# Kernel optimization log

Hardware: AMD Instinct MI355X
Metric: run time of the kernel (lower is better)

## Reference

```python
import jax, jax.numpy as jnp
import numpy as np

N_NODES = 100000


def gcn_conv(x, edge_index, W, b, n_nodes):
    # PyG GCNConv: add self-loops, symmetric normalization D^-1/2 (A+I) D^-1/2, then XW + b
    xw = x @ W  # [N, out]
    loops = jnp.arange(n_nodes, dtype=edge_index.dtype)
    src = jnp.concatenate([edge_index[0], loops])  # [E+N]
    dst = jnp.concatenate([edge_index[1], loops])
    deg = jax.ops.segment_sum(jnp.ones_like(dst, dtype=xw.dtype), dst, num_segments=n_nodes)
    dinv = jnp.where(deg > 0, deg ** -0.5, 0.0).astype(xw.dtype)
    norm = dinv[src] * dinv[dst]  # [E+N]
    msgs = xw[src] * norm[:, None]  # gather source features, scale
    out = jax.ops.segment_sum(msgs, dst, num_segments=n_nodes)  # scatter-add at dst
    return out + b


def setup_inputs() -> dict:
    key = jax.random.key(0)
    k1, k2, k3, k4 = jax.random.split(key, 4)
    F_in, dim, n_cls, n_edges = 512, 32, 40, 3200000
    x = jax.random.normal(k1, (N_NODES, F_in), dtype=jnp.float32)
    edge_index = jax.random.randint(k2, (2, n_edges), 0, N_NODES, dtype=jnp.int64)
    W1 = jax.random.normal(k3, (F_in, dim), dtype=jnp.float32) * (1.0 / np.sqrt(F_in))
    b1 = jnp.zeros((dim,), dtype=jnp.float32)
    W2 = jax.random.normal(k4, (dim, n_cls), dtype=jnp.float32) * (1.0 / np.sqrt(dim))
    b2 = jnp.zeros((n_cls,), dtype=jnp.float32)
    return {"x": x, "edge_index": edge_index, "W1": W1, "b1": b1, "W2": W2, "b2": b2}


def reference(x, edge_index, W1, b1, W2, b2):
    h = jax.nn.relu(gcn_conv(x, edge_index, W1, b1, N_NODES))
    # F.dropout with training=False (eval) is identity
    logits = gcn_conv(h, edge_index, W2, b2, N_NODES)
    return jax.nn.log_softmax(logits, axis=1)
```

## Files before the change

### kernel.cpp

```cpp
#include <hip/hip_runtime.h>
#include <hip/hip_bf16.h>
#include <math.h>


#define DIM 32
#define NCLS 40
#define F_IN 512
#define BSH 8
#define EPB 8192

__device__ __forceinline__ unsigned int bf16rne(float x) {
    unsigned int u = __float_as_uint(x);
    return (u + 0x7fffu + ((u >> 16) & 1u)) >> 16;
}
__device__ __forceinline__ unsigned int packpair(float lo, float hi) {
    return bf16rne(lo) | (bf16rne(hi) << 16);
}
__device__ __forceinline__ void unpack8(uint4 u, float* f) {
    f[0] = __uint_as_float(u.x << 16);
    f[1] = __uint_as_float(u.x & 0xffff0000u);
    f[2] = __uint_as_float(u.y << 16);
    f[3] = __uint_as_float(u.y & 0xffff0000u);
    f[4] = __uint_as_float(u.z << 16);
    f[5] = __uint_as_float(u.z & 0xffff0000u);
    f[6] = __uint_as_float(u.w << 16);
    f[7] = __uint_as_float(u.w & 0xffff0000u);
}

__global__ __launch_bounds__(256) void hist_k(const int* __restrict__ dst,
                                              int* __restrict__ gh, int E, int nbk) {
    __shared__ int h[512];
    int tid = threadIdx.x;
    h[tid] = 0; h[tid + 256] = 0;
    __syncthreads();
    int base = blockIdx.x * EPB;
#pragma unroll 4
    for (int k = 0; k < EPB / 256; ++k) {
        int e = base + k * 256 + tid;
        if (e < E) atomicAdd(&h[dst[e] >> BSH], 1);
    }
    __syncthreads();
    if (h[tid]) atomicAdd(&gh[tid], h[tid]);
    if (h[tid + 256]) atomicAdd(&gh[tid + 256], h[tid + 256]);
}

__global__ __launch_bounds__(512) void scanb_k(const int* __restrict__ gh,
                                               int* __restrict__ bbase,
                                               int* __restrict__ gcur, int nbk) {
    __shared__ int sh[512];
    int t = threadIdx.x;
    int c = (t < nbk) ? gh[t] : 0;
    sh[t] = c;
    __syncthreads();
    for (int off = 1; off < 512; off <<= 1) {
        int v = sh[t];
        if (t >= off) v += sh[t - off];
        __syncthreads();
        sh[t] = v;
        __syncthreads();
    }
    int excl = sh[t] - c;
    if (t < nbk) { bbase[t] = excl; gcur[t] = excl; }
    if (t == 0) bbase[nbk] = sh[511];
}

__global__ __launch_bounds__(256) void part_k(const int* __restrict__ src,
                                              const int* __restrict__ dst,
                                              int* __restrict__ gcur,
                                              int2* __restrict__ pairs, int E) {
    __shared__ int2 st[EPB];
    __shared__ int h[512];
    __shared__ int hb[512];
    int tid = threadIdx.x;
    h[tid] = 0; h[tid + 256] = 0;
    __syncthreads();
    int base = blockIdx.x * EPB;
#pragma unroll 4
    for (int k = 0; k < EPB / 256; ++k) {
        int e = base + k * 256 + tid;
        if (e < E) {
            int2 p; p.x = src[e]; p.y = dst[e];
            st[k * 256 + tid] = p;
            atomicAdd(&h[p.y >> BSH], 1);
        }
    }
    __syncthreads();
    for (int b = tid; b < 512; b += 256) {
        int cnt = h[b];
        hb[b] = cnt ? atomicAdd(&gcur[b], cnt) : 0;
        h[b] = 0;
    }
    __syncthreads();
#pragma unroll 4
    for (int k = 0; k < EPB / 256; ++k) {
        int e = base + k * 256 + tid;
        if (e < E) {
            int2 p = st[k * 256 + tid];
            int b = p.y >> BSH;
            int r = atomicAdd(&h[b], 1);
            pairs[hb[b] + r] = p;
        }
    }
}

__global__ __launch_bounds__(256) void build_k(const int2* __restrict__ pairs,
                                               const int* __restrict__ bbase,
                                               int* __restrict__ rowptr,
                                               int* __restrict__ csr,
                                               float* __restrict__ dinv,
                                               int n, int nbk, int E) {
    __shared__ int cnt[256];
    __shared__ int sc[256];
    __shared__ int cur[256];
    int tid = threadIdx.x;
    int b = blockIdx.x;
    int lo = bbase[b], hi = bbase[b + 1];
    cnt[tid] = 0;
    __syncthreads();
    for (int i = lo + tid; i < hi; i += 256)
        atomicAdd(&cnt[pairs[i].y & 255], 1);
    __syncthreads();
    int c = cnt[tid];
    sc[tid] = c;
    __syncthreads();
    for (int off = 1; off < 256; off <<= 1) {
        int v = sc[tid];
        if (tid >= off) v += sc[tid - off];
        __syncthreads();
        sc[tid] = v;
        __syncthreads();
    }
    int excl = sc[tid] - c;
    int v = (b << BSH) + tid;
    if (v < n) {
        rowptr[v] = lo + excl;
        dinv[v] = rsqrtf((float)(c + 1));
    }
    cur[tid] = lo + excl;
    __syncthreads();
    for (int i = lo + tid; i < hi; i += 256) {
        int2 p = pairs[i];
        int pos = atomicAdd(&cur[p.y & 255], 1);
        csr[pos] = p.x;
    }
    if (b == 0 && tid == 0) rowptr[n] = E;
}

#define GBM 64
__global__ __launch_bounds__(256) void gemm1_k(const float* __restrict__ x,
                                               const float* __restrict__ W1,
                                               const float* __restrict__ dinv,
                                               unsigned short* __restrict__ xwp, int n) {
    __shared__ float xs[32 * 68];
    __shared__ float ws[32 * 33];
    int tid = threadIdx.x;
    int base = blockIdx.x * GBM;
    int c = tid & 31;
    int rg = tid >> 5;
    float acc[8] = {0.f, 0.f, 0.f, 0.f, 0.f, 0.f, 0.f, 0.f};

    int lr = tid >> 2;
    int lq = tid & 3;
    int grow = base + lr;
    if (grow >= n) grow = n - 1;
    const float* xrow = x + (size_t)grow * F_IN;
    int wk = tid >> 3;
    int wc = tid & 7;

    for (int k0 = 0; k0 < F_IN; k0 += 32) {
        float4 a0 = *(const float4*)(xrow + k0 + lq * 4);
        float4 a1 = *(const float4*)(xrow + k0 + 16 + lq * 4);
        float4 wv = *(const float4*)(W1 + (size_t)(k0 + wk) * DIM + wc * 4);
        __syncthreads();
        xs[(lq * 4 + 0) * 68 + lr] = a0.x;
        xs[(lq * 4 + 1) * 68 + lr] = a0.y;
        xs[(lq * 4 + 2) * 68 + lr] = a0.z;
        xs[(lq * 4 + 3) * 68 + lr] = a0.w;
        xs[(lq * 4 + 16) * 68 + lr] = a1.x;
        xs[(lq * 4 + 17) * 68 + lr] = a1.y;
        xs[(lq * 4 + 18) * 68 + lr] = a1.z;
        xs[(lq * 4 + 19) * 68 + lr] = a1.w;
        ws[wk * 33 + wc * 4 + 0] = wv.x;
        ws[wk * 33 + wc * 4 + 1] = wv.y;
        ws[wk * 33 + wc * 4 + 2] = wv.z;
        ws[wk * 33 + wc * 4 + 3] = wv.w;
        __syncthreads();
#pragma unroll
        for (int kk = 0; kk < 32; ++kk) {
            float w = ws[kk * 33 + c];
            const float4 b0 = *(const float4*)&xs[kk * 68 + rg * 8];
            const float4 b1 = *(const float4*)&xs[kk * 68 + rg * 8 + 4];
            acc[0] += b0.x * w; acc[1] += b0.y * w;
            acc[2] += b0.z * w; acc[3] += b0.w * w;
            acc[4] += b1.x * w; acc[5] += b1.y * w;
            acc[6] += b1.z * w; acc[7] += b1.w * w;
        }
    }
#pragma unroll
    for (int i = 0; i < 8; ++i) {
        int row = base + rg * 8 + i;
        if (row < n)
            xwp[(size_t)row * DIM + c] = (unsigned short)bf16rne(acc[i] * dinv[row]);
    }
}

__global__ __launch_bounds__(256) void agg1_k(const uint4* __restrict__ F,
                                              const int* __restrict__ rowptr,
                                              const int* __restrict__ csr,
                                              const float* __restrict__ dinv,
                                              const float* __restrict__ bias,
                                              uint4* __restrict__ out, int n) {
    int t = blockIdx.x * 256 + threadIdx.x;
    int v = t >> 2;
    int f8 = t & 3;
    if (v >= n) return;
    float s[8], tmp[8];
    unpack8(F[(size_t)v * 4 + f8], s);
    int e = rowptr[v];
    int end = rowptr[v + 1];
    for (; e + 1 < end; e += 2) {
        int u0 = csr[e];
        int u1 = csr[e + 1];
        uint4 ua = F[(size_t)u0 * 4 + f8];
        uint4 ub = F[(size_t)u1 * 4 + f8];
        unpack8(ua, tmp);
#pragma unroll
        for (int j = 0; j < 8; ++j) s[j] += tmp[j];
        unpack8(ub, tmp);
#pragma unroll
        for (int j = 0; j < 8; ++j) s[j] += tmp[j];
    }
    if (e < end) {
        unpack8(F[(size_t)csr[e] * 4 + f8], tmp);
#pragma unroll
        for (int j = 0; j < 8; ++j) s[j] += tmp[j];
    }
    float dv = dinv[v];
    float4 b0 = *(const float4*)(bias + f8 * 8);
    float4 b1 = *(const float4*)(bias + f8 * 8 + 4);
    float bb[8] = {b0.x, b0.y, b0.z, b0.w, b1.x, b1.y, b1.z, b1.w};
    float r[8];
#pragma unroll
    for (int j = 0; j < 8; ++j) r[j] = fmaxf(s[j] * dv + bb[j], 0.f) * dv;
    uint4 o;
    o.x = packpair(r[0], r[1]);
    o.y = packpair(r[2], r[3]);
    o.z = packpair(r[4], r[5]);
    o.w = packpair(r[6], r[7]);
    out[(size_t)v * 4 + f8] = o;
}

__global__ __launch_bounds__(256) void agg2final_k(const uint4* __restrict__ F,
                                                   const int* __restrict__ rowptr,
                                                   const int* __restrict__ csr,
                                                   const float* __restrict__ dinv,
                                                   const float* __restrict__ W2,
                                                   const float* __restrict__ b2,
                                                   float* __restrict__ out, int n) {
    __shared__ float w2s[DIM * NCLS];
    __shared__ float b2s[NCLS];
    __shared__ float a2s[64 * 33];
    int tid = threadIdx.x;
    for (int i = tid; i < DIM * NCLS; i += 256) w2s[i] = W2[i];
    if (tid < NCLS) b2s[tid] = b2[tid];

    int nl = tid >> 2;
    int f8 = tid & 3;
    int v = blockIdx.x * 64 + nl;
    if (v < n) {
        float s[8], tmp[8];
        unpack8(F[(size_t)v * 4 + f8], s);
        int e = rowptr[v];
        int end = rowptr[v + 1];
        for (; e + 1 < end; e += 2) {
            int u0 = csr[e];
            int u1 = csr[e + 1];
            uint4 ua = F[(size_t)u0 * 4 + f8];
            uint4 ub = F[(size_t)u1 * 4 + f8];
            unpack8(ua, tmp);
#pragma unroll
            for (int j = 0; j < 8; ++j) s[j] += tmp[j];
            unpack8(ub, tmp);
#pragma unroll
            for (int j = 0; j < 8; ++j) s[j] += tmp[j];
        }
        if (e < end) {
            unpack8(F[(size_t)csr[e] * 4 + f8], tmp);
#pragma unroll
            for (int j = 0; j < 8; ++j) s[j] += tmp[j];
        }
        float dv = dinv[v];
#pragma unroll
        for (int j = 0; j < 8; ++j) a2s[nl * 33 + f8 * 8 + j] = s[j] * dv;
    }
    __syncthreads();

    int q = f8;
    float lg[10];
#pragma unroll
    for (int c = 0; c < 10; ++c) lg[c] = b2s[q * 10 + c];
#pragma unroll
    for (int k = 0; k < DIM; ++k) {
        float a = a2s[nl * 33 + k];
        const float* wr = &w2s[k * NCLS + q * 10];
#pragma unroll
        for (int c = 0; c < 10; ++c) lg[c] += a * wr[c];
    }
    float m = lg[0];
#pragma unroll
    for (int c = 1; c < 10; ++c) m = fmaxf(m, lg[c]);
    m = fmaxf(m, __shfl_xor(m, 1));
    m = fmaxf(m, __shfl_xor(m, 2));
    float ssum = 0.f;
#pragma unroll
    for (int c = 0; c < 10; ++c) ssum += __expf(lg[c] - m);
    ssum += __shfl_xor(ssum, 1);
    ssum += __shfl_xor(ssum, 2);
    float lse = m + __logf(ssum);
    if (v < n) {
        float* o = out + (size_t)v * NCLS + q * 10;
#pragma unroll
        for (int c = 0; c < 10; ++c) o[c] = lg[c] - lse;
    }
}

extern "C" void kernel_launch(void* const* d_in, const int* in_sizes, int n_in,
                              void* d_out, int out_size, void* d_ws, size_t ws_size,
                              hipStream_t stream) {
    const float* x  = (const float*)d_in[0];
    const int*   ei = (const int*)d_in[1];
    const float* W1 = (const float*)d_in[2];
    const float* b1 = (const float*)d_in[3];
    const float* W2 = (const float*)d_in[4];
    const float* b2 = (const float*)d_in[5];
    float* out = (float*)d_out;

    int n = in_sizes[0] / F_IN;
    int E = in_sizes[1] / 2;
    const int* src = ei;
    const int* dst = ei + E;
    int nbk = (n + 255) >> BSH;

    char* w = (char*)d_ws;
    size_t off = 0;
    auto alloc = [&](size_t bytes) -> void* {
        void* p = w + off;
        off += (bytes + 255) & ~(size_t)255;
        return p;
    };
    size_t featB2 = ((size_t)n * DIM * 2 + 255) & ~(size_t)255;
    int*   csr    = (int*)alloc((size_t)E * 4);
    char*  pairsR = (char*)alloc((size_t)E * 8);
    int*   rowptr = (int*)alloc((size_t)(n + 1) * 4);
    float* dinv   = (float*)alloc((size_t)n * 4);
    int*   gh     = (int*)alloc(512 * 4);
    int*   bbase  = (int*)alloc(513 * 4);
    int*   gcur   = (int*)alloc(512 * 4);
    (void)ws_size;

    int2*           pairs = (int2*)pairsR;
    unsigned short* xwp   = (unsigned short*)pairsR;
    unsigned short* hts   = (unsigned short*)(pairsR + featB2);

    hipMemsetAsync(gh, 0, 512 * 4, stream);

    int nebk = (E + EPB - 1) / EPB;
    hist_k <<<nebk, 256, 0, stream>>>(dst, gh, E, nbk);
    scanb_k<<<1, 512, 0, stream>>>(gh, bbase, gcur, nbk);
    part_k <<<nebk, 256, 0, stream>>>(src, dst, gcur, pairs, E);
    build_k<<<nbk, 256, 0, stream>>>(pairs, bbase, rowptr, csr, dinv, n, nbk, E);

    gemm1_k<<<(n + GBM - 1) / GBM, 256, 0, stream>>>(x, W1, dinv, xwp, n);
    agg1_k<<<((size_t)n * 4 + 255) / 256, 256, 0, stream>>>(
        (const uint4*)xwp, rowptr, csr, dinv, b1, (uint4*)hts, n);
    agg2final_k<<<(n + 63) / 64, 256, 0, stream>>>(
        (const uint4*)hts, rowptr, csr, dinv, W2, b2, out, n);
}
```

Baseline: 532.3 us.

## Pack edge pairs into 32-bit words, restructure GEMM per-row, unroll gathers by four

The partition stage now writes one 32-bit word per edge, holding the low 8 bits of the destination and a 17-bit source id, instead of an int2. This halves the traffic of the pairs buffer between partition and CSR build. gemm1 is rewritten so each thread owns one output row with 32 accumulators, reading W1 straight from global memory, and writes bf16 rows as vector stores. Both aggregation kernels unroll the neighbour gather loop by four to keep more loads in flight. The 17-bit packing assumes fewer than 131072 nodes, and the 32 accumulators per thread raise register pressure.

```diff
diff --git a/kernel.cpp b/kernel.cpp
--- a/kernel.cpp
+++ b/kernel.cpp
@@ -67,8 +67,8 @@
 __global__ __launch_bounds__(256) void part_k(const int* __restrict__ src,
                                               const int* __restrict__ dst,
                                               int* __restrict__ gcur,
-                                              int2* __restrict__ pairs, int E) {
-    __shared__ int2 st[EPB];
+                                              int* __restrict__ pairs, int E) {
+    __shared__ int st[EPB];
     __shared__ int h[512];
     __shared__ int hb[512];
     int tid = threadIdx.x;
@@ -79,9 +79,9 @@
     for (int k = 0; k < EPB / 256; ++k) {
         int e = base + k * 256 + tid;
         if (e < E) {
-            int2 p; p.x = src[e]; p.y = dst[e];
-            st[k * 256 + tid] = p;
-            atomicAdd(&h[p.y >> BSH], 1);
+            int d = dst[e];
+            st[k * 256 + tid] = d;
+            atomicAdd(&h[d >> BSH], 1);
         }
     }
     __syncthreads();
@@ -95,15 +95,15 @@
     for (int k = 0; k < EPB / 256; ++k) {
         int e = base + k * 256 + tid;
         if (e < E) {
-            int2 p = st[k * 256 + tid];
-            int b = p.y >> BSH;
+            int d = st[k * 256 + tid];
+            int b = d >> BSH;
             int r = atomicAdd(&h[b], 1);
-            pairs[hb[b] + r] = p;
-        }
-    }
-}
-
-__global__ __launch_bounds__(256) void build_k(const int2* __restrict__ pairs,
+            pairs[hb[b] + r] = ((d & 255) << 17) | src[e];
+        }
+    }
+}
+
+__global__ __launch_bounds__(256) void build_k(const int* __restrict__ pairs,
                                                const int* __restrict__ bbase,
                                                int* __restrict__ rowptr,
                                                int* __restrict__ csr,
@@ -118,7 +118,7 @@
     cnt[tid] = 0;
     __syncthreads();
     for (int i = lo + tid; i < hi; i += 256)
-        atomicAdd(&cnt[pairs[i].y & 255], 1);
+        atomicAdd(&cnt[pairs[i] >> 17], 1);
     __syncthreads();
     int c = cnt[tid];
     sc[tid] = c;
@@ -139,68 +139,61 @@
     cur[tid] = lo + excl;
     __syncthreads();
     for (int i = lo + tid; i < hi; i += 256) {
-        int2 p = pairs[i];
-        int pos = atomicAdd(&cur[p.y & 255], 1);
-        csr[pos] = p.x;
+        int p = pairs[i];
+        int pos = atomicAdd(&cur[p >> 17], 1);
+        csr[pos] = p & 0x1FFFF;
     }
     if (b == 0 && tid == 0) rowptr[n] = E;
 }
 
-#define GBM 64
+#define GROWS 256
 __global__ __launch_bounds__(256) void gemm1_k(const float* __restrict__ x,
                                                const float* __restrict__ W1,
                                                const float* __restrict__ dinv,
                                                unsigned short* __restrict__ xwp, int n) {
-    __shared__ float xs[32 * 68];
-    __shared__ float ws[32 * 33];
-    int tid = threadIdx.x;
-    int base = blockIdx.x * GBM;
-    int c = tid & 31;
-    int rg = tid >> 5;
-    float acc[8] = {0.f, 0.f, 0.f, 0.f, 0.f, 0.f, 0.f, 0.f};
-
-    int lr = tid >> 2;
-    int lq = tid & 3;
-    int grow = base + lr;
-    if (grow >= n) grow = n - 1;
-    const float* xrow = x + (size_t)grow * F_IN;
-    int wk = tid >> 3;
-    int wc = tid & 7;
+    __shared__ float xs[32 * 257];
+    int tid = threadIdx.x;
+    int base = blockIdx.x * GROWS;
+    float acc[DIM];
+#pragma unroll
+    for (int c = 0; c < DIM; ++c) acc[c] = 0.f;
+    int q = tid & 7;
+    int r0 = tid >> 3;
 
     for (int k0 = 0; k0 < F_IN; k0 += 32) {
-        float4 a0 = *(const float4*)(xrow + k0 + lq * 4);
-        float4 a1 = *(const float4*)(xrow + k0 + 16 + lq * 4);
-        float4 wv = *(const float4*)(W1 + (size_t)(k0 + wk) * DIM + wc * 4);
-        __syncthreads();
-        xs[(lq * 4 + 0) * 68 + lr] = a0.x;
-        xs[(lq * 4 + 1) * 68 + lr] = a0.y;
-        xs[(lq * 4 + 2) * 68 + lr] = a0.z;
-        xs[(lq * 4 + 3) * 68 + lr] = a0.w;
-        xs[(lq * 4 + 16) * 68 + lr] = a1.x;
-        xs[(lq * 4 + 17) * 68 + lr] = a1.y;
-        xs[(lq * 4 + 18) * 68 + lr] = a1.z;
-        xs[(lq * 4 + 19) * 68 + lr] = a1.w;
-        ws[wk * 33 + wc * 4 + 0] = wv.x;
-        ws[wk * 33 + wc * 4 + 1] = wv.y;
-        ws[wk * 33 + wc * 4 + 2] = wv.z;
-        ws[wk * 33 + wc * 4 + 3] = wv.w;
-        __syncthreads();
-#pragma unroll
+        __syncthreads();
+#pragma unroll
+        for (int pass = 0; pass < 8; ++pass) {
+            int r = r0 + pass * 32;
+            int grow = base + r;
+            if (grow >= n) grow = n - 1;
+            float4 a = *(const float4*)(x + (size_t)grow * F_IN + k0 + q * 4);
+            xs[(q * 4 + 0) * 257 + r] = a.x;
+            xs[(q * 4 + 1) * 257 + r] = a.y;
+            xs[(q * 4 + 2) * 257 + r] = a.z;
+            xs[(q * 4 + 3) * 257 + r] = a.w;
+        }
+        __syncthreads();
+        const float* wr = W1 + (size_t)k0 * DIM;
+#pragma unroll 4
         for (int kk = 0; kk < 32; ++kk) {
-            float w = ws[kk * 33 + c];
-            const float4 b0 = *(const float4*)&xs[kk * 68 + rg * 8];
-            const float4 b1 = *(const float4*)&xs[kk * 68 + rg * 8 + 4];
-            acc[0] += b0.x * w; acc[1] += b0.y * w;
-            acc[2] += b0.z * w; acc[3] += b0.w * w;
-            acc[4] += b1.x * w; acc[5] += b1.y * w;
-            acc[6] += b1.z * w; acc[7] += b1.w * w;
-        }
-    }
-#pragma unroll
-    for (int i = 0; i < 8; ++i) {
-        int row = base + rg * 8 + i;
-        if (row < n)
-            xwp[(size_t)row * DIM + c] = (unsigned short)bf16rne(acc[i] * dinv[row]);
+            float xv = xs[kk * 257 + tid];
+#pragma unroll
+            for (int c = 0; c < DIM; ++c)
+                acc[c] = fmaf(wr[kk * DIM + c], xv, acc[c]);
+        }
+    }
+    int row = base + tid;
+    if (row < n) {
+        float dv = dinv[row];
+        uint4 o[4];
+        unsigned int* po = (unsigned int*)o;
+#pragma unroll
+        for (int j = 0; j < 16; ++j)
+            po[j] = packpair(acc[2 * j] * dv, acc[2 * j + 1] * dv);
+        uint4* d4 = (uint4*)(xwp + (size_t)row * DIM);
+#pragma unroll
+        for (int j = 0; j < 4; ++j) d4[j] = o[j];
     }
 }
 
@@ -218,19 +211,25 @@
     unpack8(F[(size_t)v * 4 + f8], s);
     int e = rowptr[v];
     int end = rowptr[v + 1];
-    for (; e + 1 < end; e += 2) {
-        int u0 = csr[e];
-        int u1 = csr[e + 1];
-        uint4 ua = F[(size_t)u0 * 4 + f8];
-        uint4 ub = F[(size_t)u1 * 4 + f8];
+    for (; e + 3 < end; e += 4) {
+        uint4 ua = F[(size_t)csr[e] * 4 + f8];
+        uint4 ub = F[(size_t)csr[e + 1] * 4 + f8];
+        uint4 uc = F[(size_t)csr[e + 2] * 4 + f8];
+        uint4 ud = F[(size_t)csr[e + 3] * 4 + f8];
         unpack8(ua, tmp);
 #pragma unroll
         for (int j = 0; j < 8; ++j) s[j] += tmp[j];
         unpack8(ub, tmp);
 #pragma unroll
         for (int j = 0; j < 8; ++j) s[j] += tmp[j];
-    }
-    if (e < end) {
+        unpack8(uc, tmp);
+#pragma unroll
+        for (int j = 0; j < 8; ++j) s[j] += tmp[j];
+        unpack8(ud, tmp);
+#pragma unroll
+        for (int j = 0; j < 8; ++j) s[j] += tmp[j];
+    }
+    for (; e < end; ++e) {
         unpack8(F[(size_t)csr[e] * 4 + f8], tmp);
 #pragma unroll
         for (int j = 0; j < 8; ++j) s[j] += tmp[j];
@@ -272,19 +271,25 @@
         unpack8(F[(size_t)v * 4 + f8], s);
         int e = rowptr[v];
         int end = rowptr[v + 1];
-        for (; e + 1 < end; e += 2) {
-            int u0 = csr[e];
-            int u1 = csr[e + 1];
-            uint4 ua = F[(size_t)u0 * 4 + f8];
-            uint4 ub = F[(size_t)u1 * 4 + f8];
+        for (; e + 3 < end; e += 4) {
+            uint4 ua = F[(size_t)csr[e] * 4 + f8];
+            uint4 ub = F[(size_t)csr[e + 1] * 4 + f8];
+            uint4 uc = F[(size_t)csr[e + 2] * 4 + f8];
+            uint4 ud = F[(size_t)csr[e + 3] * 4 + f8];
             unpack8(ua, tmp);
 #pragma unroll
             for (int j = 0; j < 8; ++j) s[j] += tmp[j];
             unpack8(ub, tmp);
 #pragma unroll
             for (int j = 0; j < 8; ++j) s[j] += tmp[j];
-        }
-        if (e < end) {
+            unpack8(uc, tmp);
+#pragma unroll
+            for (int j = 0; j < 8; ++j) s[j] += tmp[j];
+            unpack8(ud, tmp);
+#pragma unroll
+            for (int j = 0; j < 8; ++j) s[j] += tmp[j];
+        }
+        for (; e < end; ++e) {
             unpack8(F[(size_t)csr[e] * 4 + f8], tmp);
 #pragma unroll
             for (int j = 0; j < 8; ++j) s[j] += tmp[j];
@@ -350,7 +355,7 @@
     };
     size_t featB2 = ((size_t)n * DIM * 2 + 255) & ~(size_t)255;
     int*   csr    = (int*)alloc((size_t)E * 4);
-    char*  pairsR = (char*)alloc((size_t)E * 8);
+    char*  pairsR = (char*)alloc((size_t)E * 4);
     int*   rowptr = (int*)alloc((size_t)(n + 1) * 4);
     float* dinv   = (float*)alloc((size_t)n * 4);
     int*   gh     = (int*)alloc(512 * 4);
@@ -358,7 +363,7 @@
     int*   gcur   = (int*)alloc(512 * 4);
     (void)ws_size;
 
-    int2*           pairs = (int2*)pairsR;
+    int*            pairs = (int*)pairsR;
     unsigned short* xwp   = (unsigned short*)pairsR;
     unsigned short* hts   = (unsigned short*)(pairsR + featB2);
 
@@ -370,7 +375,7 @@
     part_k <<<nebk, 256, 0, stream>>>(src, dst, gcur, pairs, E);
     build_k<<<nbk, 256, 0, stream>>>(pairs, bbase, rowptr, csr, dinv, n, nbk, E);
 
-    gemm1_k<<<(n + GBM - 1) / GBM, 256, 0, stream>>>(x, W1, dinv, xwp, n);
+    gemm1_k<<<(n + GROWS - 1) / GROWS, 256, 0, stream>>>(x, W1, dinv, xwp, n);
     agg1_k<<<((size_t)n * 4 + 255) / 256, 256, 0, stream>>>(
         (const uint4*)xwp, rowptr, csr, dinv, b1, (uint4*)hts, n);
     agg2final_k<<<(n + 63) / 64, 256, 0, stream>>>(
```

Result: slower. 640.6 us (+20.4%).
